# Kernel tuning notes

Hardware: AMD Instinct MI355X
Metric: run time of the kernel (lower is better)

The kernel has to match this reference:

```python
import jax, jax.numpy as jnp
import numpy as np

LAPLACIAN = jnp.array([[-1., -1., -1.], [-1., 8., -1.], [-1., -1., -1.]], dtype=jnp.float32).reshape(1, 1, 3, 3)
AVG5 = jnp.ones((1, 1, 5, 5), dtype=jnp.float32) / 25.0


def _conv_same(x, kernel):
    # x: [B,1,H,W], kernel: [O=1,I=1,kh,kw], SAME padding (odd kernels)
    return jax.lax.conv_general_dilated(
        x, kernel, window_strides=(1, 1), padding='SAME',
        dimension_numbers=('NCHW', 'OIHW', 'NCHW'))


def setup_inputs() -> dict:
    key = jax.random.key(0)
    k0, k1, k2, k3 = jax.random.split(key, 4)
    B, H, W = 16, 1024, 1024
    mask = jax.random.uniform(k0, (B, 1, H, W), dtype=jnp.float32)
    # per-sample params scaled into documented ranges
    blur_strength = 1.0 + 4.0 * jax.random.uniform(k1, (B, 1), dtype=jnp.float32)      # 1.0-5.0
    edge_sensitivity = 0.5 + 1.5 * jax.random.uniform(k2, (B, 1), dtype=jnp.float32)   # 0.5-2.0
    final_threshold = 0.3 + 0.4 * jax.random.uniform(k3, (B, 1), dtype=jnp.float32)    # 0.3-0.7
    return {"mask": mask, "blur_strength": blur_strength,
            "edge_sensitivity": edge_sensitivity, "final_threshold": final_threshold}


def reference(mask, blur_strength, edge_sensitivity, final_threshold):
    B = mask.shape[0]
    edges = jnp.abs(_conv_same(mask, LAPLACIAN))                      # [B,1,H,W]
    edge_threshold = 0.5 * edge_sensitivity.reshape(B, 1, 1, 1)
    edge_mask = (edges > edge_threshold).astype(mask.dtype)
    smoothed_base = _conv_same(mask, AVG5)                            # 5x5 box blur
    blur_factor = blur_strength.reshape(B, 1, 1, 1) / 3.0
    smoothed = mask * (1.0 - blur_factor) + smoothed_base * blur_factor
    result = mask * (1.0 - edge_mask) + smoothed * edge_mask
    final_mask = (result > final_threshold.reshape(B, 1, 1, 1)).astype(mask.dtype)
    return final_mask
```

## Files before the change

### kernel.cpp

```cpp
#include <hip/hip_runtime.h>

#define NB 16
#define HH 1024
#define WW 1024
#define TW 128
#define TH 32
#define LC 136
#define LR 36
#define N4 (LR * (LC / 4))
#define NSTG 5

#define EPS1 2e-4f
#define EPS2 1e-4f

typedef float f32x4 __attribute__((ext_vector_type(4)));
typedef float f32x2 __attribute__((ext_vector_type(2)));

__device__ __noinline__ float aes_exact(const float (*raw)[LC], int lr, int lc,
                                        float bsf, float esf, float fthr)
{
    const double bfd   = (double)bsf / 3.0;
    const double ethrd = 0.5 * (double)esf;
    const double fthrd = (double)fthr;
    const double w25d  = (double)(1.0f / 25.0f);

    double s25 = 0.0, s9 = 0.0;
    for (int dy = 0; dy < 5; ++dy)
        for (int dx = 0; dx < 5; ++dx) {
            double v = (double)raw[lr + dy][lc + dx];
            s25 += v;
            if (dy >= 1 && dy <= 3 && dx >= 1 && dx <= 3) s9 += v;
        }
    double c      = (double)raw[lr + 2][lc + 2];
    double edges  = fabs(9.0 * c - s9);
    double sbase  = s25 * w25d;
    double smooth = c * (1.0 - bfd) + sbase * bfd;
    double result = (edges > ethrd) ? smooth : c;
    return (result > fthrd) ? 1.0f : 0.0f;
}

__global__ __launch_bounds__(256, 4)
void aes_kernel(const float* __restrict__ mask,
                const float* __restrict__ blur_strength,
                const float* __restrict__ edge_sensitivity,
                const float* __restrict__ final_threshold,
                float* __restrict__ out)
{
    __shared__ float raw[2][LR][LC];

    const int b      = blockIdx.z;
    const int tile_y = blockIdx.y * TH;
    const int tx0    = blockIdx.x * (2 * TW);
    const float* m = mask + (size_t)b * (HH * WW);

    const float bsf    = blur_strength[b];
    const float esf    = edge_sensitivity[b];
    const float fthr   = final_threshold[b];
    const float ethr   = 0.5f * esf;
    const float bff    = bsf / 3.0f;
    const float onembf = 1.0f - bff;
    const float w25f   = 1.0f / 25.0f;

    const int tx  = threadIdx.x & 31;
    const int ty  = threadIdx.x >> 5;
    const int lr0 = ty * 4;
    const int lc0 = 4 * tx + 2;

    f32x4 stg[NSTG];

#define STAGE_LOAD(TILE_X)                                                  \
    {                                                                       \
        _Pragma("unroll")                                                   \
        for (int k = 0; k < NSTG; ++k) {                                    \
            int i = (int)threadIdx.x + k * 256;                             \
            f32x4 v = {0.f, 0.f, 0.f, 0.f};                                 \
            if (i < N4) {                                                   \
                int row = i / (LC / 4);                                     \
                int c4  = i - row * (LC / 4);                               \
                int gy  = tile_y - 2 + row;                                 \
                int gx  = (TILE_X) - 4 + 4 * c4;           \
                if ((unsigned)gy < (unsigned)HH && (unsigned)gx < (unsigned)WW) \
                    v = *(const f32x4*)(m + (size_t)gy * WW + gx);          \
            }                                                               \
            stg[k] = v;                                                     \
        }                                                                   \
    }

#define STAGE_WRITE(BUF)                                                    \
    {                                                                       \
        _Pragma("unroll")                                                   \
        for (int k = 0; k < NSTG; ++k) {                                    \
            int i = (int)threadIdx.x + k * 256;                             \
            if (i < N4) {                                                   \
                int row = i / (LC / 4);                                     \
                int c4  = i - row * (LC / 4);                               \
                *(f32x4*)&raw[(BUF)][row][4 * c4] = stg[k];                 \
            }                                                               \
        }                                                                   \
    }

#define LOADROWV(RB, ROWIDX, K)                                             \
    {                                                                       \
        const float* rp = &RB[(ROWIDX)][0];                                 \
        f32x2 u0 = *(const f32x2*)(rp + lc0);                    \
        f32x4 u1 = *(const f32x4*)(rp + lc0 + 2);               \
        f32x2 u2 = *(const f32x2*)(rp + lc0 + 6);                \
        f32x4 A = {u0.x, u0.y, u1.x, u1.y};                                 \
        f32x4 B = {u0.y, u1.x, u1.y, u1.z};                                 \
        f32x4 D = {u1.y, u1.z, u1.w, u2.x};                                 \
        f32x4 E = {u1.z, u1.w, u2.x, u2.y};                                 \
        f32x4 h3v = (B + D) + u1;                                           \
        h3r[(K)] = h3v;                                                     \
        h5r[(K)] = (A + E) + h3v;                                           \
        ccr[(K)] = u1;                                                      \
    }

#define COMPUTE(BUF, TILE_X)                                                \
    {                                                                       \
        const float (*rb)[LC] = raw[(BUF)];                                 \
        f32x4 h5r[5], h3r[5], ccr[5];                                       \
        _Pragma("unroll")                                                   \
        for (int k = 0; k < 4; ++k)                                         \
            LOADROWV(rb, lr0 + k, k)                                        \
        f32x4 S25 = (h5r[0] + h5r[1]) + (h5r[2] + h5r[3]);      \
        float* op = out + (size_t)b * (HH * WW)                             \
                        + (size_t)(tile_y + ty * 4) * WW + (TILE_X) + 4 * tx; \
        _Pragma("unroll")                                                   \
        for (int r = 0; r < 4; ++r) {                                       \
            LOADROWV(rb, lr0 + r + 4, (r + 4) % 5)                          \
            const int i1 = (r + 1) % 5, i2 = (r + 2) % 5, i3 = (r + 3) % 5; \
            const int i4 = (r + 4) % 5;                                     \
            f32x4 S25f = S25 + h5r[i4];                                     \
            f32x4 S9   = (h3r[i1] + h3r[i3]) + h3r[i2];                     \
            f32x4 cc   = ccr[i2];                                           \
            f32x4 e    = cc * 9.0f - S9;                        \
            f32x4 sb   = S25f * w25f;                                       \
            f32x4 sm   = cc * onembf + sb * bff;         \
            f32x4 d2   = sm - fthr;                                         \
            f32x4 ov;                                                       \
            _Pragma("unroll")                                               \
            for (int c = 0; c < 4; ++c) {                                   \
                float ec  = fabsf(e[c]);                         \
                float dd1 = ec - ethr;                                      \
                bool isedge = dd1 > 0.0f;                                   \
                bool conf = (fabsf(dd1) > EPS1) &&                          \
                            (!isedge || (fabsf(d2[c]) > EPS2));             \
                bool hit = isedge ? (d2[c] > 0.0f) : (cc[c] > fthr);        \
                float o  = hit ? 1.0f : 0.0f;                               \
                if (!conf)                                                  \
                    o = aes_exact(rb, lr0 + r, lc0 + c, bsf, esf, fthr);    \
                ov[c] = o;                                                  \
            }                                                               \
            __builtin_nontemporal_store(ov, (f32x4*)(op + (size_t)r * WW)); \
            if (r < 3) S25 = S25f - h5r[r % 5];      \
        }                                                                   \
    }

    STAGE_LOAD(tx0)
    STAGE_WRITE(0)
    __syncthreads();

    STAGE_LOAD(tx0 + TW)
    COMPUTE(0, tx0)
    STAGE_WRITE(1)
    __syncthreads();

    COMPUTE(1, tx0 + TW)

#undef STAGE_LOAD
#undef STAGE_WRITE
#undef LOADROWV
#undef COMPUTE
}

extern "C" void kernel_launch(void* const* d_in, const int* in_sizes, int n_in,
                              void* d_out, int out_size, void* d_ws, size_t ws_size,
                              hipStream_t stream) {
    const float* mask = (const float*)d_in[0];
    const float* bs   = (const float*)d_in[1];
    const float* es   = (const float*)d_in[2];
    const float* ft   = (const float*)d_in[3];
    float* out = (float*)d_out;

    dim3 grid(WW / (2 * TW), HH / TH, NB);
    aes_kernel<<<grid, 256, 0, stream>>>(mask, bs, es, ft, out);
}
```

Before: 34.57 us.

## Give each wavefront its own LDS strip and drop block barriers

Each 64-lane wavefront now owns a private LDS region covering a 64-column by 16-row output sub-tile plus halo. It walks four such sub-tiles down a 64-row strip, prefetching the next sub-tile into registers while computing the current one. Blocks shrink to 128 threads and all __syncthreads calls are removed, relying on in-order LDS access within a single wavefront. The aim is to cut barrier stalls and improve latency hiding. In exchange, halo redundancy rises because of the narrower columns and shorter row chunks.

```diff
diff --git a/kernel.cpp b/kernel.cpp
--- a/kernel.cpp
+++ b/kernel.cpp
@@ -3,12 +3,15 @@
 #define NB 16
 #define HH 1024
 #define WW 1024
-#define TW 128
-#define TH 32
-#define LC 136
-#define LR 36
-#define N4 (LR * (LC / 4))
-#define NSTG 5
+#define BW 128
+#define BH 64
+#define WVT 4
+#define STH 16
+#define SLR 20
+#define SLC 72
+#define SQ4 (SLC / 4)
+#define NEL (SLR * SQ4)
+#define NLD 6
 
 #define EPS1 2e-4f
 #define EPS2 1e-4f
@@ -16,7 +19,7 @@
 typedef float f32x4 __attribute__((ext_vector_type(4)));
 typedef float f32x2 __attribute__((ext_vector_type(2)));
 
-__device__ __noinline__ float aes_exact(const float (*raw)[LC], int lr, int lc,
+__device__ __noinline__ float aes_exact(const float (*raw)[SLC], int lr, int lc,
                                         float bsf, float esf, float fthr)
 {
     const double bfd   = (double)bsf / 3.0;
@@ -39,18 +42,17 @@
     return (result > fthrd) ? 1.0f : 0.0f;
 }
 
-__global__ __launch_bounds__(256, 4)
+__global__ __launch_bounds__(128)
 void aes_kernel(const float* __restrict__ mask,
                 const float* __restrict__ blur_strength,
                 const float* __restrict__ edge_sensitivity,
                 const float* __restrict__ final_threshold,
                 float* __restrict__ out)
 {
-    __shared__ float raw[2][LR][LC];
+    __shared__ float region[2][SLR][SLC];
 
-    const int b      = blockIdx.z;
-    const int tile_y = blockIdx.y * TH;
-    const int tx0    = blockIdx.x * (2 * TW);
+    const int b       = blockIdx.z;
+    const int strip_y = blockIdx.y * BH;
     const float* m = mask + (size_t)b * (HH * WW);
 
     const float bsf    = blur_strength[b];
@@ -61,24 +63,29 @@
     const float onembf = 1.0f - bff;
     const float w25f   = 1.0f / 25.0f;
 
-    const int tx  = threadIdx.x & 31;
-    const int ty  = threadIdx.x >> 5;
-    const int lr0 = ty * 4;
-    const int lc0 = 4 * tx + 2;
+    const int lane = threadIdx.x & 63;
+    const int wv   = threadIdx.x >> 6;
+    const int wxb  = blockIdx.x * BW + wv * 64;
 
-    f32x4 stg[NSTG];
+    const int cg  = lane & 15;
+    const int rg  = lane >> 4;
+    const int lr0 = rg * 4;
+    const int lc0 = 4 * cg + 2;
 
-#define STAGE_LOAD(TILE_X)                                                  \
+    float (*reg_)[SLC] = region[wv];
+    f32x4 stg[NLD];
+
+#define LOADREGS(T)                                                         \
     {                                                                       \
+        const int gy0 = strip_y + (T) * STH - 2;                            \
         _Pragma("unroll")                                                   \
-        for (int k = 0; k < NSTG; ++k) {                                    \
-            int i = (int)threadIdx.x + k * 256;                             \
+        for (int k = 0; k < NLD; ++k) {                                     \
+            int i = lane + k * 64;                                          \
             f32x4 v = {0.f, 0.f, 0.f, 0.f};                                 \
-            if (i < N4) {                                                   \
-                int row = i / (LC / 4);                                     \
-                int c4  = i - row * (LC / 4);                               \
-                int gy  = tile_y - 2 + row;                                 \
-                int gx  = (TILE_X) - 4 + 4 * c4;           \
+            if (i < NEL) {                                                  \
+                int row = i / SQ4, q = i - row * SQ4;                       \
+                int gy = gy0 + row;                                         \
+                int gx = wxb - 4 + 4 * q;                  \
                 if ((unsigned)gy < (unsigned)HH && (unsigned)gx < (unsigned)WW) \
                     v = *(const f32x4*)(m + (size_t)gy * WW + gx);          \
             }                                                               \
@@ -86,22 +93,21 @@
         }                                                                   \
     }
 
-#define STAGE_WRITE(BUF)                                                    \
+#define WRITELDS()                                                          \
     {                                                                       \
         _Pragma("unroll")                                                   \
-        for (int k = 0; k < NSTG; ++k) {                                    \
-            int i = (int)threadIdx.x + k * 256;                             \
-            if (i < N4) {                                                   \
-                int row = i / (LC / 4);                                     \
-                int c4  = i - row * (LC / 4);                               \
-                *(f32x4*)&raw[(BUF)][row][4 * c4] = stg[k];                 \
+        for (int k = 0; k < NLD; ++k) {                                     \
+            int i = lane + k * 64;                                          \
+            if (i < NEL) {                                                  \
+                int row = i / SQ4, q = i - row * SQ4;                       \
+                *(f32x4*)&reg_[row][4 * q] = stg[k];                        \
             }                                                               \
         }                                                                   \
     }
 
-#define LOADROWV(RB, ROWIDX, K)                                             \
+#define LOADROWV(ROWIDX, K)                                                 \
     {                                                                       \
-        const float* rp = &RB[(ROWIDX)][0];                                 \
+        const float* rp = &reg_[(ROWIDX)][0];                               \
         f32x2 u0 = *(const f32x2*)(rp + lc0);                    \
         f32x4 u1 = *(const f32x4*)(rp + lc0 + 2);               \
         f32x2 u2 = *(const f32x2*)(rp + lc0 + 6);                \
@@ -115,32 +121,31 @@
         ccr[(K)] = u1;                                                      \
     }
 
-#define COMPUTE(BUF, TILE_X)                                                \
+#define COMPUTE(T)                                                          \
     {                                                                       \
-        const float (*rb)[LC] = raw[(BUF)];                                 \
         f32x4 h5r[5], h3r[5], ccr[5];                                       \
         _Pragma("unroll")                                                   \
         for (int k = 0; k < 4; ++k)                                         \
-            LOADROWV(rb, lr0 + k, k)                                        \
-        f32x4 S25 = (h5r[0] + h5r[1]) + (h5r[2] + h5r[3]);      \
+            LOADROWV(lr0 + k, k)                                            \
+        f32x4 S25 = (h5r[0] + h5r[1]) + (h5r[2] + h5r[3]);                  \
         float* op = out + (size_t)b * (HH * WW)                             \
-                        + (size_t)(tile_y + ty * 4) * WW + (TILE_X) + 4 * tx; \
+                  + (size_t)(strip_y + (T) * STH + lr0) * WW + wxb + 4 * cg;\
         _Pragma("unroll")                                                   \
         for (int r = 0; r < 4; ++r) {                                       \
-            LOADROWV(rb, lr0 + r + 4, (r + 4) % 5)                          \
+            LOADROWV(lr0 + r + 4, (r + 4) % 5)                              \
             const int i1 = (r + 1) % 5, i2 = (r + 2) % 5, i3 = (r + 3) % 5; \
             const int i4 = (r + 4) % 5;                                     \
             f32x4 S25f = S25 + h5r[i4];                                     \
             f32x4 S9   = (h3r[i1] + h3r[i3]) + h3r[i2];                     \
             f32x4 cc   = ccr[i2];                                           \
-            f32x4 e    = cc * 9.0f - S9;                        \
+            f32x4 e    = cc * 9.0f - S9;                                    \
             f32x4 sb   = S25f * w25f;                                       \
-            f32x4 sm   = cc * onembf + sb * bff;         \
+            f32x4 sm   = cc * onembf + sb * bff;                            \
             f32x4 d2   = sm - fthr;                                         \
             f32x4 ov;                                                       \
             _Pragma("unroll")                                               \
             for (int c = 0; c < 4; ++c) {                                   \
-                float ec  = fabsf(e[c]);                         \
+                float ec  = fabsf(e[c]);                                    \
                 float dd1 = ec - ethr;                                      \
                 bool isedge = dd1 > 0.0f;                                   \
                 bool conf = (fabsf(dd1) > EPS1) &&                          \
@@ -148,27 +153,26 @@
                 bool hit = isedge ? (d2[c] > 0.0f) : (cc[c] > fthr);        \
                 float o  = hit ? 1.0f : 0.0f;                               \
                 if (!conf)                                                  \
-                    o = aes_exact(rb, lr0 + r, lc0 + c, bsf, esf, fthr);    \
+                    o = aes_exact(reg_, lr0 + r, lc0 + c, bsf, esf, fthr);  \
                 ov[c] = o;                                                  \
             }                                                               \
             __builtin_nontemporal_store(ov, (f32x4*)(op + (size_t)r * WW)); \
-            if (r < 3) S25 = S25f - h5r[r % 5];      \
+            if (r < 3) S25 = S25f - h5r[r % 5];                             \
         }                                                                   \
     }
 
-    STAGE_LOAD(tx0)
-    STAGE_WRITE(0)
-    __syncthreads();
+    LOADREGS(0)
+    WRITELDS()
 
-    STAGE_LOAD(tx0 + TW)
-    COMPUTE(0, tx0)
-    STAGE_WRITE(1)
-    __syncthreads();
+    #pragma unroll
+    for (int t = 0; t < WVT; ++t) {
+        if (t < WVT - 1) LOADREGS(t + 1)
+        COMPUTE(t)
+        if (t < WVT - 1) WRITELDS()
+    }
 
-    COMPUTE(1, tx0 + TW)
-
-#undef STAGE_LOAD
-#undef STAGE_WRITE
+#undef LOADREGS
+#undef WRITELDS
 #undef LOADROWV
 #undef COMPUTE
 }
@@ -182,6 +186,6 @@
     const float* ft   = (const float*)d_in[3];
     float* out = (float*)d_out;
 
-    dim3 grid(WW / (2 * TW), HH / TH, NB);
-    aes_kernel<<<grid, 256, 0, stream>>>(mask, bs, es, ft, out);
+    dim3 grid(WW / BW, HH / BH, NB);
+    aes_kernel<<<grid, 128, 0, stream>>>(mask, bs, es, ft, out);
 }
```

Result: slower. 38.36 us (+11.0%).
